# Optimization experiments

Hardware: AMD Instinct MI355X
Metric: run time of the kernel (lower is better)

The kernel has to match this reference:

```python
import jax, jax.numpy as jnp
import numpy as np

D_MODEL = 1024
N_HEADS = 16
D_HEAD = D_MODEL // N_HEADS
HIDDEN = 4 * D_MODEL
EPS = 1e-5
ROPE_BASE = 10000.0


def layernorm(x, g, b):
    mu = jnp.mean(x, axis=-1, keepdims=True)
    var = jnp.mean((x - mu) ** 2, axis=-1, keepdims=True)
    return (x - mu) * jax.lax.rsqrt(var + EPS) * g + b


def rope(t, pos):
    # t: (B, N, D), pos: (N,) int -> rotary transform over D (half-split pairs)
    half = t.shape[-1] // 2
    inv_freq = 1.0 / (ROPE_BASE ** (jnp.arange(half, dtype=jnp.float32) / half))
    ang = pos.astype(jnp.float32)[:, None] * inv_freq  # (N, half)
    cos, sin = jnp.cos(ang), jnp.sin(ang)
    t1, t2 = t[..., :half], t[..., half:]
    return jnp.concatenate([t1 * cos - t2 * sin, t1 * sin + t2 * cos], axis=-1)


def setup_inputs() -> dict:
    key = jax.random.key(0)
    ks = jax.random.split(key, 12)
    B, N, D, H = 2, 2048, D_MODEL, HIDDEN
    s = 0.02
    return {
        "x": jax.random.normal(ks[0], (B, N, D), jnp.float32),
        "pos": jnp.arange(N, dtype=jnp.int32),
        "Wq": jax.random.normal(ks[1], (D, D), jnp.float32) * s,
        "bq": jnp.zeros((D,), jnp.float32),
        "Wk": jax.random.normal(ks[2], (D, D), jnp.float32) * s,
        "bk": jnp.zeros((D,), jnp.float32),
        "Wv": jax.random.normal(ks[3], (D, D), jnp.float32) * s,
        "bv": jnp.zeros((D,), jnp.float32),
        "Wo": jax.random.normal(ks[4], (D, D), jnp.float32) * s,
        "bo": jnp.zeros((D,), jnp.float32),
        "g1": jnp.ones((D,), jnp.float32),
        "b1": jnp.zeros((D,), jnp.float32),
        "g2": jnp.ones((D,), jnp.float32),
        "b2": jnp.zeros((D,), jnp.float32),
        "W1": jax.random.normal(ks[5], (D, H), jnp.float32) * s,
        "bm1": jnp.zeros((H,), jnp.float32),
        "W2": jax.random.normal(ks[6], (H, D), jnp.float32) * s,
        "bm2": jnp.zeros((D,), jnp.float32),
    }


def reference(x, pos, Wq, bq, Wk, bk, Wv, bv, Wo, bo, g1, b1, g2, b2, W1, bm1, W2, bm2):
    B, N, D = x.shape
    Hh, dh = N_HEADS, D_HEAD

    # --- attention sublayer (pre-norm) ---
    h = layernorm(x, g1, b1)
    q = h @ Wq + bq
    k = h @ Wk + bk
    v = h @ Wv + bv
    q = rope(q, pos)
    k = rope(k, pos)
    # split heads: (B, Hh, N, dh)
    q = q.reshape(B, N, Hh, dh).transpose(0, 2, 1, 3)
    k = k.reshape(B, N, Hh, dh).transpose(0, 2, 1, 3)
    v = v.reshape(B, N, Hh, dh).transpose(0, 2, 1, 3)
    scores = jnp.einsum("bhqd,bhkd->bhqk", q, k) / jnp.sqrt(jnp.float32(dh))
    attn = jax.nn.softmax(scores, axis=-1)
    ctx = jnp.einsum("bhqk,bhkd->bhqd", attn, v)
    ctx = ctx.transpose(0, 2, 1, 3).reshape(B, N, D)
    x = x + ctx @ Wo + bo

    # --- MLP sublayer (pre-norm, exact GELU) ---
    h = layernorm(x, g2, b2)
    h = jax.nn.gelu(h @ W1 + bm1, approximate=False)
    x = x + h @ W2 + bm2
    return x
```

## Files before the change

kernel.cpp:

```cpp
#include <hip/hip_runtime.h>

typedef __bf16 bf16x8 __attribute__((ext_vector_type(8)));
typedef __bf16 bf16x4 __attribute__((ext_vector_type(4)));
typedef float  f32x4  __attribute__((ext_vector_type(4)));

#define D_MODEL 1024
#define SEQ     2048
#define BATCH   2
#define NH      16
#define DH      64
#define HID     4096
#define ROWS    (BATCH*SEQ)

static __device__ __forceinline__ void gl_lds16(const __bf16* g, __bf16* l) {
  __builtin_amdgcn_global_load_lds(
      (const __attribute__((address_space(1))) unsigned int*)g,
      (__attribute__((address_space(3))) unsigned int*)l, 16, 0, 0);
}

__global__ __launch_bounds__(256) void ln_kernel(
    const float* __restrict__ x, const float* __restrict__ g,
    const float* __restrict__ b, __bf16* __restrict__ out)
{
  int row = blockIdx.x;
  const float* xr = x + (size_t)row * D_MODEL;
  int i0 = threadIdx.x * 4;
  f32x4 xv = *(const f32x4*)(xr + i0);
  float s  = xv[0] + xv[1] + xv[2] + xv[3];
  float ss = xv[0]*xv[0] + xv[1]*xv[1] + xv[2]*xv[2] + xv[3]*xv[3];
#pragma unroll
  for (int off = 1; off < 64; off <<= 1) {
    s  += __shfl_xor(s,  off, 64);
    ss += __shfl_xor(ss, off, 64);
  }
  __shared__ float red[8];
  int wave = threadIdx.x >> 6;
  if ((threadIdx.x & 63) == 0) { red[wave] = s; red[4 + wave] = ss; }
  __syncthreads();
  s  = red[0] + red[1] + red[2] + red[3];
  ss = red[4] + red[5] + red[6] + red[7];
  float mu  = s * (1.0f / D_MODEL);
  float var = ss * (1.0f / D_MODEL) - mu * mu;
  float inv = rsqrtf(var + 1e-5f);
  f32x4 gv = *(const f32x4*)(g + i0);
  f32x4 bv = *(const f32x4*)(b + i0);
  bf16x4 ov;
#pragma unroll
  for (int j = 0; j < 4; ++j)
    ov[j] = (__bf16)((xv[j] - mu) * inv * gv[j] + bv[j]);
  *(bf16x4*)(out + (size_t)row * D_MODEL + i0) = ov;
}

__global__ __launch_bounds__(256) void convT_kernel(
    const float* __restrict__ W, __bf16* __restrict__ Wt, int K, int N)
{
  __shared__ float T[32][33];
  int n0 = blockIdx.x * 32, k0 = blockIdx.y * 32;
  int r  = threadIdx.x >> 3;
  int c4 = (threadIdx.x & 7) * 4;
  f32x4 v = *(const f32x4*)(W + (size_t)(k0 + r) * N + n0 + c4);
#pragma unroll
  for (int i = 0; i < 4; ++i) T[r][c4 + i] = v[i];
  __syncthreads();
  bf16x4 o;
#pragma unroll
  for (int i = 0; i < 4; ++i) o[i] = (__bf16)T[c4 + i][r];
  *(bf16x4*)(Wt + (size_t)(n0 + r) * K + k0 + c4) = o;
}

__global__ void biascat_kernel(const float* __restrict__ a,
                               const float* __restrict__ b,
                               const float* __restrict__ c,
                               float* __restrict__ o)
{
  int i = blockIdx.x * 256 + threadIdx.x;
  o[i] = i < 1024 ? a[i] : (i < 2048 ? b[i - 1024] : c[i - 2048]);
}

__global__ __launch_bounds__(256) void gemm128(
    const __bf16* __restrict__ A, const __bf16* __restrict__ Bt,
    const float* __restrict__ bias, const float* __restrict__ resid,
    void* __restrict__ Cv, int M, int N, int K, int act, int c_fp32)
{
  __shared__ __bf16 As[128 * 64];
  __shared__ __bf16 Bs[128 * 64];
  int tid = threadIdx.x, lane = tid & 63, wv = tid >> 6;
  int quad = lane >> 4, l16 = lane & 15;
  int wr = wv >> 1, wc = wv & 1;
  int gx = M >> 7, gy = N >> 7;
  int blk = blockIdx.x;
  int xcd = blk & 7, t = blk >> 3;
  int row0 = (t % gx) * 128;
  int col0 = (xcd * (gy >> 3) + t / gx) * 128;
  int s_r8 = lane >> 3;
  int s_c8 = lane & 7;
  int s_src = (s_c8 ^ s_r8) * 8;
  int sw = l16 & 7;
  f32x4 acc[4][4] = {};

  for (int k0 = 0; k0 < K; k0 += 64) {
#pragma unroll
    for (int p = 0; p < 4; ++p) {
      int r = p * 32 + wv * 8 + s_r8;
      gl_lds16(A  + (size_t)(row0 + r) * K + k0 + s_src, As + p * 2048 + wv * 512);
      gl_lds16(Bt + (size_t)(col0 + r) * K + k0 + s_src, Bs + p * 2048 + wv * 512);
    }
    __syncthreads();
#pragma unroll
    for (int kk = 0; kk < 2; ++kk) {
      int slot = ((kk * 4 + quad) ^ sw) * 8;
      bf16x8 af[4], bf[4];
#pragma unroll
      for (int i = 0; i < 4; ++i) {
        af[i] = *(const bf16x8*)(As + (wr * 64 + i * 16 + l16) * 64 + slot);
        bf[i] = *(const bf16x8*)(Bs + (wc * 64 + i * 16 + l16) * 64 + slot);
      }
#pragma unroll
      for (int i = 0; i < 4; ++i)
#pragma unroll
        for (int j = 0; j < 4; ++j)
          acc[i][j] = __builtin_amdgcn_mfma_f32_16x16x32_bf16(af[i], bf[j], acc[i][j], 0, 0, 0);
    }
    __syncthreads();
  }
#pragma unroll
  for (int i = 0; i < 4; ++i) {
    int grow = row0 + wr * 64 + i * 16 + quad * 4;
#pragma unroll
    for (int j = 0; j < 4; ++j) {
      int gcol = col0 + wc * 64 + j * 16 + l16;
      float bsv = bias[gcol];
#pragma unroll
      for (int r = 0; r < 4; ++r) {
        size_t off = (size_t)(grow + r) * N + gcol;
        float v = acc[i][j][r] + bsv;
        if (act) v = 0.5f * v * (1.0f + erff(v * 0.70710678118654752f));
        if (resid) v += resid[off];
        if (c_fp32) ((float*)Cv)[off] = v;
        else        ((__bf16*)Cv)[off] = (__bf16)v;
      }
    }
  }
}

__global__ __launch_bounds__(256) void gemm64x128(
    const __bf16* __restrict__ A, const __bf16* __restrict__ Bt,
    const float* __restrict__ bias, const float* __restrict__ resid,
    void* __restrict__ Cv, int M, int N, int K, int act, int c_fp32)
{
  __shared__ __bf16 As[64 * 64];
  __shared__ __bf16 Bs[128 * 64];
  int tid = threadIdx.x, lane = tid & 63, wv = tid >> 6;
  int quad = lane >> 4, l16 = lane & 15;
  int wr = wv >> 1, wc = wv & 1;
  int gx = M >> 6, gy = N >> 7;
  int blk = blockIdx.x;
  int xcd = blk & 7, t = blk >> 3;
  int row0 = (t % gx) * 64;
  int col0 = (xcd * (gy >> 3) + t / gx) * 128;
  int s_r8 = lane >> 3;
  int s_c8 = lane & 7;
  int s_src = (s_c8 ^ s_r8) * 8;
  int sw = l16 & 7;
  f32x4 acc[2][4] = {};

  for (int k0 = 0; k0 < K; k0 += 64) {
#pragma unroll
    for (int p = 0; p < 4; ++p) {
      int r = p * 32 + wv * 8 + s_r8;
      if (p < 2)
        gl_lds16(A + (size_t)(row0 + r) * K + k0 + s_src, As + p * 2048 + wv * 512);
      gl_lds16(Bt + (size_t)(col0 + r) * K + k0 + s_src, Bs + p * 2048 + wv * 512);
    }
    __syncthreads();
#pragma unroll
    for (int kk = 0; kk < 2; ++kk) {
      int slot = ((kk * 4 + quad) ^ sw) * 8;
      bf16x8 af[2], bf[4];
#pragma unroll
      for (int i = 0; i < 2; ++i)
        af[i] = *(const bf16x8*)(As + (wr * 32 + i * 16 + l16) * 64 + slot);
#pragma unroll
      for (int j = 0; j < 4; ++j)
        bf[j] = *(const bf16x8*)(Bs + (wc * 64 + j * 16 + l16) * 64 + slot);
#pragma unroll
      for (int i = 0; i < 2; ++i)
#pragma unroll
        for (int j = 0; j < 4; ++j)
          acc[i][j] = __builtin_amdgcn_mfma_f32_16x16x32_bf16(af[i], bf[j], acc[i][j], 0, 0, 0);
    }
    __syncthreads();
  }
#pragma unroll
  for (int i = 0; i < 2; ++i) {
    int grow = row0 + wr * 32 + i * 16 + quad * 4;
#pragma unroll
    for (int j = 0; j < 4; ++j) {
      int gcol = col0 + wc * 64 + j * 16 + l16;
      float bsv = bias[gcol];
#pragma unroll
      for (int r = 0; r < 4; ++r) {
        size_t off = (size_t)(grow + r) * N + gcol;
        float v = acc[i][j][r] + bsv;
        if (act) v = 0.5f * v * (1.0f + erff(v * 0.70710678118654752f));
        if (resid) v += resid[off];
        if (c_fp32) ((float*)Cv)[off] = v;
        else        ((__bf16*)Cv)[off] = (__bf16)v;
      }
    }
  }
}

__global__ __launch_bounds__(256) void rope_repack(
    const __bf16* __restrict__ qkv, const int* __restrict__ pos,
    __bf16* __restrict__ Qh, __bf16* __restrict__ Kh)
{
  int row = blockIdx.x;
  int b = row >> 11, n = row & (SEQ - 1);
  float p = (float)pos[n];
  const __bf16* qr = qkv + (size_t)row * 3072;
#pragma unroll
  for (int t = 0; t < 2; ++t) {
    int i = threadIdx.x + t * 256;
    float fr  = expf(-9.210340371976184f * ((float)i * (1.0f / 512.0f)));
    float ang = p * fr;
    float sn, c;
    sincosf(ang, &sn, &c);
    float q1 = (float)qr[i],        q2 = (float)qr[512 + i];
    float k1 = (float)qr[1024 + i], k2 = (float)qr[1536 + i];
    int h1 = i >> 6, d1 = i & 63;
    int h2 = (i + 512) >> 6;
    size_t o1 = ((size_t)(b * NH + h1) * SEQ + n) * DH + d1;
    size_t o2 = ((size_t)(b * NH + h2) * SEQ + n) * DH + d1;
    Qh[o1] = (__bf16)((q1 * c - q2 * sn) * 0.125f);
    Qh[o2] = (__bf16)((q1 * sn + q2 * c) * 0.125f);
    Kh[o1] = (__bf16)(k1 * c - k2 * sn);
    Kh[o2] = (__bf16)(k1 * sn + k2 * c);
  }
}

__global__ __launch_bounds__(256) void vtrans_kernel(
    const __bf16* __restrict__ Vsrc, int vstride, __bf16* __restrict__ Vt,
    int blocked)
{
  __shared__ __bf16 T[64][72];
  int bh = blockIdx.x;
  int kb = blockIdx.y * 64;
  int b = bh >> 4, h = bh & 15;
  int tid = threadIdx.x;
#pragma unroll
  for (int t = 0; t < 2; ++t) {
    int u = tid + t * 256;
    int r = u >> 3, seg = (u & 7) * 8;
    bf16x8 v = *(const bf16x8*)(Vsrc + (size_t)(b * SEQ + kb + r) * vstride + h * DH + seg);
    *(bf16x8*)(&T[r][seg]) = v;
  }
  __syncthreads();
#pragma unroll
  for (int t = 0; t < 2; ++t) {
    int u = tid + t * 256;
    int d = u >> 3, ks = (u & 7) * 8;
    bf16x8 o;
#pragma unroll
    for (int i = 0; i < 8; ++i) o[i] = T[ks + i][d];
    if (blocked) {
      int key = kb + ks;
      *(bf16x8*)(Vt + (((size_t)bh * (SEQ / 128) + (key >> 7)) * DH + d) * 128 + (key & 127)) = o;
    } else {
      *(bf16x8*)(Vt + ((size_t)bh * DH + d) * SEQ + kb + ks) = o;
    }
  }
}

#define KS 136
__global__ __launch_bounds__(256) void attn_split(
    const __bf16* __restrict__ Qh, const __bf16* __restrict__ Kh,
    const __bf16* __restrict__ Vt, __bf16* __restrict__ pacc,
    float* __restrict__ pml)
{
  __shared__ __bf16 Ks[128 * 64];
  __shared__ __bf16 Vs[64 * 128];
  __shared__ __bf16 Pl[4][16 * KS];
  int tid = threadIdx.x, lane = tid & 63, wave = tid >> 6;
  int quad = lane >> 4, l16 = lane & 15;
  int blk = blockIdx.x;
  int split = blk >> 10;
  int rr = blk & 1023;
  int bh  = ((rr & 7) << 2) | ((rr >> 3) & 3);
  int q64 = rr >> 5;
  int q0 = q64 * 64 + wave * 16;
  const __bf16* qbase = Qh + (size_t)bh * SEQ * DH;
  const __bf16* kbase = Kh + (size_t)bh * SEQ * DH;
  const __bf16* vbase = Vt + (size_t)bh * SEQ * DH;
  const __bf16* qp = qbase + (size_t)(q0 + l16) * DH + quad * 8;
  bf16x8 qf0 = *(const bf16x8*)(qp);
  bf16x8 qf1 = *(const bf16x8*)(qp + 32);
  float lrow[4] = {0.f, 0.f, 0.f, 0.f};
  f32x4 acc[4] = {};
  __bf16* pw = &Pl[wave][0];
  int s_kr = lane >> 3;
  int s_k8 = lane & 7;
  int s_vd = lane >> 4;
  int s_vs = lane & 15;
  int sw8  = l16 & 7;

  int kb0 = split * (SEQ / 2);
  for (int it = 0; it < (SEQ / 2) / 128; ++it) {
    int kb = kb0 + it * 128;
    const __bf16* kt = kbase + (size_t)kb * DH;
    const __bf16* vt = vbase + (size_t)(kb >> 7) * (DH * 128);
    __syncthreads();
#pragma unroll
    for (int p = 0; p < 4; ++p) {
      int key0 = p * 32 + wave * 8;
      int swz  = (key0 >> 3) & 7;
      gl_lds16(kt + (key0 + s_kr) * DH + ((s_k8 ^ swz) * 8), Ks + p * 2048 + wave * 512);
      int d = p * 16 + wave * 4 + s_vd;
      gl_lds16(vt + d * 128 + ((s_vs ^ (d & 15)) * 8), Vs + p * 2048 + wave * 512);
    }
    __syncthreads();
    f32x4 s[8];
#pragma unroll
    for (int j = 0; j < 8; ++j) {
      const __bf16* kr = Ks + (l16 * 8 + j) * 64;
      bf16x8 kf0 = *(const bf16x8*)(kr + (quad ^ sw8) * 8);
      bf16x8 kf1 = *(const bf16x8*)(kr + ((quad ^ sw8) ^ 4) * 8);
      f32x4 z = {};
      z = __builtin_amdgcn_mfma_f32_16x16x32_bf16(qf0, kf0, z, 0, 0, 0);
      s[j] = __builtin_amdgcn_mfma_f32_16x16x32_bf16(qf1, kf1, z, 0, 0, 0);
    }
#pragma unroll
    for (int r = 0; r < 4; ++r) {
      bf16x8 pv;
      float rs = 0.f;
#pragma unroll
      for (int j = 0; j < 8; ++j) {
        float pj = __expf(s[j][r]);
        rs += pj;
        pv[j] = (__bf16)pj;
      }
      lrow[r] += rs;
      *(bf16x8*)(pw + (quad * 4 + r) * KS + l16 * 8) = pv;
    }
#pragma unroll
    for (int kk = 0; kk < 4; ++kk) {
      bf16x8 pf = *(const bf16x8*)(pw + l16 * KS + kk * 32 + quad * 8);
#pragma unroll
      for (int j = 0; j < 4; ++j) {
        int d = j * 16 + l16;
        bf16x8 vf = *(const bf16x8*)(Vs + d * 128 + (((kk * 4 + quad) ^ (d & 15)) * 8));
        acc[j] = __builtin_amdgcn_mfma_f32_16x16x32_bf16(pf, vf, acc[j], 0, 0, 0);
      }
    }
  }
#pragma unroll
  for (int r = 0; r < 4; ++r)
#pragma unroll
    for (int off = 1; off < 16; off <<= 1) lrow[r] += __shfl_xor(lrow[r], off, 64);
#pragma unroll
  for (int r = 0; r < 4; ++r) {
    int brow = wave * 16 + quad * 4 + r;
#pragma unroll
    for (int j = 0; j < 4; ++j)
      pacc[((size_t)blk * 64 + brow) * 64 + j * 16 + l16] = (__bf16)acc[j][r];
    if (l16 == 0) {
      pml[(size_t)blk * 128 + brow]      = 0.f;
      pml[(size_t)blk * 128 + 64 + brow] = lrow[r];
    }
  }
}

__global__ __launch_bounds__(256) void attn_combine(
    const __bf16* __restrict__ pacc, const float* __restrict__ pml,
    __bf16* __restrict__ ctx)
{
  int bq = blockIdx.x;
  int q64 = bq & 31, bh = bq >> 5;
  int b = bh >> 4, h = bh & 15;
  int tid = threadIdx.x;
  int r = tid >> 2;
  int c = (tid & 3) * 16;
  int blk0 = ((q64 * 4 + (bh & 3)) << 3) | (bh >> 2);
  int blk1 = blk0 + 1024;
  float m0 = pml[(size_t)blk0 * 128 + r], l0 = pml[(size_t)blk0 * 128 + 64 + r];
  float m1 = pml[(size_t)blk1 * 128 + r], l1 = pml[(size_t)blk1 * 128 + 64 + r];
  float m = fmaxf(m0, m1);
  float w0 = __expf(m0 - m), w1 = __expf(m1 - m);
  float inv = 1.0f / (w0 * l0 + w1 * l1);
  size_t r0 = ((size_t)blk0 * 64 + r) * 64 + c;
  size_t r1 = ((size_t)blk1 * 64 + r) * 64 + c;
  size_t ob = ((size_t)(b * SEQ) + q64 * 64 + r) * D_MODEL + h * DH + c;
#pragma unroll
  for (int g = 0; g < 2; ++g) {
    bf16x8 a0 = *(const bf16x8*)(pacc + r0 + g * 8);
    bf16x8 a1 = *(const bf16x8*)(pacc + r1 + g * 8);
    bf16x8 o;
#pragma unroll
    for (int i = 0; i < 8; ++i)
      o[i] = (__bf16)((w0 * (float)a0[i] + w1 * (float)a1[i]) * inv);
    *(bf16x8*)(ctx + ob + g * 8) = o;
  }
}

__global__ __launch_bounds__(256) void rope_inplace(
    __bf16* __restrict__ ql, __bf16* __restrict__ kl,
    const int* __restrict__ pos, int stride)
{
  int row = blockIdx.x;
  int n = row & (SEQ - 1);
  float p = (float)pos[n];
  const size_t rbase = (size_t)row * stride;
#pragma unroll
  for (int t = 0; t < 2; ++t) {
    int i = threadIdx.x + t * 256;
    float fr  = expf(-9.210340371976184f * ((float)i * (1.0f / 512.0f)));
    float ang = p * fr;
    float sn, c;
    sincosf(ang, &sn, &c);
    float q1 = (float)ql[rbase + i], q2 = (float)ql[rbase + 512 + i];
    float k1 = (float)kl[rbase + i], k2 = (float)kl[rbase + 512 + i];
    ql[rbase + i]       = (__bf16)(q1 * c - q2 * sn);
    ql[rbase + 512 + i] = (__bf16)(q1 * sn + q2 * c);
    kl[rbase + i]       = (__bf16)(k1 * c - k2 * sn);
    kl[rbase + 512 + i] = (__bf16)(k1 * sn + k2 * c);
  }
}

__global__ __launch_bounds__(256) void attn_kernel(
    const __bf16* __restrict__ Q, const __bf16* __restrict__ K,
    const __bf16* __restrict__ Vt, __bf16* __restrict__ ctx, int qkstride)
{
  __shared__ __bf16 Pl[4][16 * KS];
  int tid = threadIdx.x, lane = tid & 63, wave = tid >> 6;
  int quad = lane >> 4, l16 = lane & 15;
  int blk = blockIdx.x;
  int q64 = blk & 31;
  int bh  = blk >> 5;
  int b = bh >> 4, h = bh & 15;
  int q0 = q64 * 64 + wave * 16;
  const __bf16* qbase = Q + (size_t)b * SEQ * qkstride + h * DH;
  const __bf16* kbase = K + (size_t)b * SEQ * qkstride + h * DH;
  const __bf16* vbase = Vt + (size_t)bh * DH * SEQ;
  const __bf16* qp = qbase + (size_t)(q0 + l16) * qkstride + quad * 8;
  bf16x8 qf0 = *(const bf16x8*)(qp);
  bf16x8 qf1 = *(const bf16x8*)(qp + 32);
  float mrow[4] = {-1e30f, -1e30f, -1e30f, -1e30f};
  float lrow[4] = {0.f, 0.f, 0.f, 0.f};
  f32x4 acc[4] = {};
  __bf16* pw = &Pl[wave][0];

  for (int kb = 0; kb < SEQ; kb += 128) {
    f32x4 s[8];
#pragma unroll
    for (int j = 0; j < 8; ++j) {
      const __bf16* kp = kbase + (size_t)(kb + l16 * 8 + j) * qkstride + quad * 8;
      bf16x8 kf0 = *(const bf16x8*)(kp);
      bf16x8 kf1 = *(const bf16x8*)(kp + 32);
      f32x4 z = {};
      z = __builtin_amdgcn_mfma_f32_16x16x32_bf16(qf0, kf0, z, 0, 0, 0);
      z = __builtin_amdgcn_mfma_f32_16x16x32_bf16(qf1, kf1, z, 0, 0, 0);
#pragma unroll
      for (int r = 0; r < 4; ++r) s[j][r] = z[r] * 0.125f;
    }
#pragma unroll
    for (int r = 0; r < 4; ++r) {
      float mx = s[0][r];
#pragma unroll
      for (int j = 1; j < 8; ++j) mx = fmaxf(mx, s[j][r]);
#pragma unroll
      for (int off = 1; off < 16; off <<= 1) mx = fmaxf(mx, __shfl_xor(mx, off, 64));
      float mn = fmaxf(mrow[r], mx);
      float al = __expf(mrow[r] - mn);
      float p[8], rs = 0.f;
#pragma unroll
      for (int j = 0; j < 8; ++j) { p[j] = __expf(s[j][r] - mn); rs += p[j]; }
#pragma unroll
      for (int off = 1; off < 16; off <<= 1) rs += __shfl_xor(rs, off, 64);
      lrow[r] = lrow[r] * al + rs;
      mrow[r] = mn;
#pragma unroll
      for (int j = 0; j < 4; ++j) acc[j][r] *= al;
      bf16x8 pv;
#pragma unroll
      for (int j = 0; j < 8; ++j) pv[j] = (__bf16)p[j];
      *(bf16x8*)(pw + (quad * 4 + r) * KS + l16 * 8) = pv;
    }
#pragma unroll
    for (int kk = 0; kk < 4; ++kk) {
      bf16x8 pf = *(const bf16x8*)(pw + l16 * KS + kk * 32 + quad * 8);
#pragma unroll
      for (int j = 0; j < 4; ++j) {
        bf16x8 vf = *(const bf16x8*)(vbase + (size_t)(j * 16 + l16) * SEQ + kb + kk * 32 + quad * 8);
        acc[j] = __builtin_amdgcn_mfma_f32_16x16x32_bf16(pf, vf, acc[j], 0, 0, 0);
      }
    }
  }
#pragma unroll
  for (int r = 0; r < 4; ++r) {
    int row = q0 + quad * 4 + r;
    float inv = 1.0f / lrow[r];
    size_t obase = ((size_t)(b * SEQ) + row) * D_MODEL + h * DH;
#pragma unroll
    for (int j = 0; j < 4; ++j)
      ctx[obase + j * 16 + l16] = (__bf16)(acc[j][r] * inv);
  }
}

extern "C" void kernel_launch(void* const* d_in, const int* in_sizes, int n_in,
                              void* d_out, int out_size, void* d_ws, size_t ws_size,
                              hipStream_t stream)
{
  const float* x   = (const float*)d_in[0];
  const int*   pos = (const int*)  d_in[1];
  const float* Wq  = (const float*)d_in[2];
  const float* bq  = (const float*)d_in[3];
  const float* Wk  = (const float*)d_in[4];
  const float* bk  = (const float*)d_in[5];
  const float* Wv  = (const float*)d_in[6];
  const float* bv  = (const float*)d_in[7];
  const float* Wo  = (const float*)d_in[8];
  const float* bo  = (const float*)d_in[9];
  const float* g1  = (const float*)d_in[10];
  const float* b1  = (const float*)d_in[11];
  const float* g2  = (const float*)d_in[12];
  const float* b2  = (const float*)d_in[13];
  const float* W1  = (const float*)d_in[14];
  const float* bm1 = (const float*)d_in[15];
  const float* W2  = (const float*)d_in[16];
  const float* bm2 = (const float*)d_in[17];
  float* out = (float*)d_out;

  const size_t MB = 1024 * 1024;
  char* w = (char*)d_ws;
  dim3 blk(256);
  dim3 gConvD(D_MODEL / 32, D_MODEL / 32);
  dim3 gConv1(HID / 32, D_MODEL / 32);
  dim3 gConv2(D_MODEL / 32, HID / 32);
  dim3 gVt(BATCH * NH, SEQ / 64);

  if (ws_size >= (size_t)96 * MB) {
    __bf16* hln   = (__bf16*)(w + 0 * MB);
    float*  x1    = (float*) (w + 8 * MB);
    __bf16* qkv   = (__bf16*)(w + 24 * MB);
    __bf16* pacc  = (__bf16*)(w + 24 * MB);
    float*  pml   = (float*) (w + 41 * MB);
    __bf16* hmlp  = (__bf16*)(w + 24 * MB);
    __bf16* Qh    = (__bf16*)(w + 48 * MB);
    __bf16* ctx   = (__bf16*)(w + 48 * MB);
    __bf16* Kh    = (__bf16*)(w + 56 * MB);
    __bf16* W2T   = (__bf16*)(w + 56 * MB);
    __bf16* Vt    = (__bf16*)(w + 64 * MB);
    __bf16* W1T   = (__bf16*)(w + 64 * MB);
    __bf16* WqkvT = (__bf16*)(w + 72 * MB);
    __bf16* WoT   = (__bf16*)(w + 78 * MB);
    float*  bqkv  = (float*) (w + 80 * MB);

    convT_kernel<<<gConvD, blk, 0, stream>>>(Wq, WqkvT,               D_MODEL, D_MODEL);
    convT_kernel<<<gConvD, blk, 0, stream>>>(Wk, WqkvT + 1024 * 1024, D_MODEL, D_MODEL);
    convT_kernel<<<gConvD, blk, 0, stream>>>(Wv, WqkvT + 2048 * 1024, D_MODEL, D_MODEL);
    convT_kernel<<<gConvD, blk, 0, stream>>>(Wo, WoT, D_MODEL, D_MODEL);
    biascat_kernel<<<12, blk, 0, stream>>>(bq, bk, bv, bqkv);
    ln_kernel<<<ROWS, blk, 0, stream>>>(x, g1, b1, hln);
    gemm128<<<(ROWS / 128) * (3072 / 128), blk, 0, stream>>>(hln, WqkvT, bqkv, nullptr, qkv, ROWS, 3072, D_MODEL, 0, 0);
    rope_repack<<<ROWS, blk, 0, stream>>>(qkv, pos, Qh, Kh);
    vtrans_kernel<<<gVt, blk, 0, stream>>>(qkv + 2048, 3072, Vt, 1);
    attn_split<<<BATCH * NH * (SEQ / 64) * 2, blk, 0, stream>>>(Qh, Kh, Vt, pacc, pml);
    attn_combine<<<BATCH * NH * (SEQ / 64), blk, 0, stream>>>(pacc, pml, ctx);
    convT_kernel<<<gConv1, blk, 0, stream>>>(W1, W1T, D_MODEL, HID);
    convT_kernel<<<gConv2, blk, 0, stream>>>(W2, W2T, HID, D_MODEL);
    gemm64x128<<<(ROWS / 64) * (D_MODEL / 128), blk, 0, stream>>>(ctx, WoT, bo, x, x1, ROWS, D_MODEL, D_MODEL, 0, 1);
    ln_kernel<<<ROWS, blk, 0, stream>>>(x1, g2, b2, hln);
    gemm128<<<(ROWS / 128) * (HID / 128), blk, 0, stream>>>(hln, W1T, bm1, nullptr, hmlp, ROWS, HID, D_MODEL, 1, 0);
    gemm64x128<<<(ROWS / 64) * (D_MODEL / 128), blk, 0, stream>>>(hmlp, W2T, bm2, x1, out, ROWS, D_MODEL, HID, 0, 1);
  } else {
    __bf16* hln  = (__bf16*)(w + 0 * MB);
    __bf16* vlin = (__bf16*)(w + 8 * MB);
    __bf16* WqT  = (__bf16*)(w + 16 * MB);
    __bf16* WkT  = (__bf16*)(w + 18 * MB);
    __bf16* WvT  = (__bf16*)(w + 20 * MB);
    __bf16* ctx  = (__bf16*)(w + 16 * MB);
    __bf16* WoT  = (__bf16*)(w + 8 * MB);
    __bf16* W1T  = (__bf16*)(w + 8 * MB);
    __bf16* W2T  = (__bf16*)(w + 16 * MB);
    __bf16* Vt   = (__bf16*)(w + 24 * MB);
    __bf16* hmlp = (__bf16*)(w + 24 * MB);
    __bf16* qlin = (__bf16*)d_out;
    __bf16* klin = (__bf16*)d_out + (size_t)ROWS * D_MODEL;
    float*  x1   = (float*)d_out;

    convT_kernel<<<gConvD, blk, 0, stream>>>(Wq, WqT, D_MODEL, D_MODEL);
    convT_kernel<<<gConvD, blk, 0, stream>>>(Wk, WkT, D_MODEL, D_MODEL);
    convT_kernel<<<gConvD, blk, 0, stream>>>(Wv, WvT, D_MODEL, D_MODEL);
    ln_kernel<<<ROWS, blk, 0, stream>>>(x, g1, b1, hln);
    int nLin = (ROWS / 64) * (D_MODEL / 128);
    gemm64x128<<<nLin, blk, 0, stream>>>(hln, WqT, bq, nullptr, qlin, ROWS, D_MODEL, D_MODEL, 0, 0);
    gemm64x128<<<nLin, blk, 0, stream>>>(hln, WkT, bk, nullptr, klin, ROWS, D_MODEL, D_MODEL, 0, 0);
    gemm64x128<<<nLin, blk, 0, stream>>>(hln, WvT, bv, nullptr, vlin, ROWS, D_MODEL, D_MODEL, 0, 0);
    rope_inplace<<<ROWS, blk, 0, stream>>>(qlin, klin, pos, D_MODEL);
    vtrans_kernel<<<gVt, blk, 0, stream>>>(vlin, D_MODEL, Vt, 0);
    attn_kernel<<<BATCH * NH * (SEQ / 64), blk, 0, stream>>>(qlin, klin, Vt, ctx, D_MODEL);
    convT_kernel<<<gConvD, blk, 0, stream>>>(Wo, WoT, D_MODEL, D_MODEL);
    gemm64x128<<<nLin, blk, 0, stream>>>(ctx, WoT, bo, x, x1, ROWS, D_MODEL, D_MODEL, 0, 1);
    ln_kernel<<<ROWS, blk, 0, stream>>>(x1, g2, b2, hln);
    convT_kernel<<<gConv1, blk, 0, stream>>>(W1, W1T, D_MODEL, HID);
    convT_kernel<<<gConv2, blk, 0, stream>>>(W2, W2T, HID, D_MODEL);
    const int CH = 1024;
    for (int c = 0; c < ROWS / CH; ++c) {
      const __bf16* a1 = hln + (size_t)c * CH * D_MODEL;
      gemm128<<<(CH / 128) * (HID / 128), blk, 0, stream>>>(a1, W1T, bm1, nullptr, hmlp, CH, HID, D_MODEL, 1, 0);
      gemm64x128<<<(CH / 64) * (D_MODEL / 128), blk, 0, stream>>>(hmlp, W2T, bm2, x1 + (size_t)c * CH * D_MODEL,
                                          out + (size_t)c * CH * D_MODEL, CH, D_MODEL, HID, 0, 1);
    }
  }
}
```

Before: 438.4 us.

## Add double-buffered 256x256 GEMM kernel for QKV and MLP projections

Introduces a 512-thread GEMM with 256x256 output tiles, double-buffered LDS staging through direct global-to-LDS loads, and a chiplet-aware block remapping. The QKV, W1 and W2 projections now use it instead of the 128-tile kernels. Larger tiles raise operand reuse and cut global traffic, while the double buffering overlaps loads with MFMA work. The cost is fewer workgroups: the W2 GEMM launches only 64 blocks on a 256-CU device, which underfills the machine. High register use from 32 accumulators per thread may also limit occupancy.

```diff
diff --git a/kernel.cpp b/kernel.cpp
--- a/kernel.cpp
+++ b/kernel.cpp
@@ -75,6 +75,94 @@
 {
   int i = blockIdx.x * 256 + threadIdx.x;
   o[i] = i < 1024 ? a[i] : (i < 2048 ? b[i - 1024] : c[i - 2048]);
+}
+
+__global__ __launch_bounds__(512, 2) void gemm256(
+    const __bf16* __restrict__ A, const __bf16* __restrict__ Bt,
+    const float* __restrict__ bias, const float* __restrict__ resid,
+    void* __restrict__ Cv, int M, int N, int K, int act, int c_fp32)
+{
+  __shared__ __bf16 As[2][256 * 64];
+  __shared__ __bf16 Bs[2][256 * 64];
+  int tid = threadIdx.x, lane = tid & 63, wv = tid >> 6;
+  int quad = lane >> 4, l16 = lane & 15;
+  int wr = wv >> 2, wc = wv & 3;
+  int gx = M >> 8, gy = N >> 8;
+  int nwg = gx * gy;
+  int xcd = blockIdx.x & 7;
+  int q = nwg >> 3, r8 = nwg & 7;
+  int wg = (xcd < r8 ? xcd * (q + 1) : r8 * (q + 1) + (xcd - r8) * q) + (blockIdx.x >> 3);
+  int row0 = (wg % gx) << 8;
+  int col0 = (wg / gx) << 8;
+  int s_r  = lane >> 3;
+  int s_src = ((lane & 7) ^ s_r) * 8;
+  int sw = l16 & 7;
+  int NT = K >> 6;
+  f32x4 acc[8][4] = {};
+
+#define G256_STAGE(kt, b)                                                     \
+  {                                                                           \
+    int k0_ = (kt) * 64;                                                      \
+    _Pragma("unroll")                                                         \
+    for (int rd = 0; rd < 4; ++rd) {                                          \
+      int rrow = rd * 64 + wv * 8 + s_r;                                      \
+      gl_lds16(A  + (size_t)(row0 + rrow) * K + k0_ + s_src,                  \
+               &As[b][rd * 4096 + wv * 512]);                                 \
+      gl_lds16(Bt + (size_t)(col0 + rrow) * K + k0_ + s_src,                  \
+               &Bs[b][rd * 4096 + wv * 512]);                                 \
+    }                                                                         \
+  }
+
+  G256_STAGE(0, 0);
+  G256_STAGE(1, 1);
+
+  for (int t = 0; t < NT; ++t) {
+    if (t + 1 < NT) asm volatile("s_waitcnt vmcnt(8)" ::: "memory");
+    else            asm volatile("s_waitcnt vmcnt(0)" ::: "memory");
+    __builtin_amdgcn_s_barrier();
+    const __bf16* Ab = &As[t & 1][0];
+    const __bf16* Bb = &Bs[t & 1][0];
+    __builtin_amdgcn_s_setprio(1);
+#pragma unroll
+    for (int kk = 0; kk < 2; ++kk) {
+      int slot = ((kk * 4 + quad) ^ sw) * 8;
+      bf16x8 bfr[4];
+#pragma unroll
+      for (int j = 0; j < 4; ++j)
+        bfr[j] = *(const bf16x8*)(Bb + (wc * 64 + j * 16 + l16) * 64 + slot);
+      bf16x8 afr[8];
+#pragma unroll
+      for (int i = 0; i < 8; ++i)
+        afr[i] = *(const bf16x8*)(Ab + (wr * 128 + i * 16 + l16) * 64 + slot);
+#pragma unroll
+      for (int i = 0; i < 8; ++i)
+#pragma unroll
+        for (int j = 0; j < 4; ++j)
+          acc[i][j] = __builtin_amdgcn_mfma_f32_16x16x32_bf16(afr[i], bfr[j], acc[i][j], 0, 0, 0);
+    }
+    __builtin_amdgcn_s_setprio(0);
+    __builtin_amdgcn_s_barrier();
+    if (t + 2 < NT) G256_STAGE(t + 2, t & 1);
+  }
+
+#pragma unroll
+  for (int i = 0; i < 8; ++i) {
+    int grow = row0 + wr * 128 + i * 16 + quad * 4;
+#pragma unroll
+    for (int j = 0; j < 4; ++j) {
+      int gcol = col0 + wc * 64 + j * 16 + l16;
+      float bsv = bias[gcol];
+#pragma unroll
+      for (int r = 0; r < 4; ++r) {
+        size_t off = (size_t)(grow + r) * N + gcol;
+        float v = acc[i][j][r] + bsv;
+        if (act) v = 0.5f * v * (1.0f + erff(v * 0.70710678118654752f));
+        if (resid) v += resid[off];
+        if (c_fp32) ((float*)Cv)[off] = v;
+        else        ((__bf16*)Cv)[off] = (__bf16)v;
+      }
+    }
+  }
 }
 
 __global__ __launch_bounds__(256) void gemm128(
@@ -533,6 +621,7 @@
   const size_t MB = 1024 * 1024;
   char* w = (char*)d_ws;
   dim3 blk(256);
+  dim3 blk512(512);
   dim3 gConvD(D_MODEL / 32, D_MODEL / 32);
   dim3 gConv1(HID / 32, D_MODEL / 32);
   dim3 gConv2(D_MODEL / 32, HID / 32);
@@ -561,7 +650,7 @@
     convT_kernel<<<gConvD, blk, 0, stream>>>(Wo, WoT, D_MODEL, D_MODEL);
     biascat_kernel<<<12, blk, 0, stream>>>(bq, bk, bv, bqkv);
     ln_kernel<<<ROWS, blk, 0, stream>>>(x, g1, b1, hln);
-    gemm128<<<(ROWS / 128) * (3072 / 128), blk, 0, stream>>>(hln, WqkvT, bqkv, nullptr, qkv, ROWS, 3072, D_MODEL, 0, 0);
+    gemm256<<<(ROWS / 256) * (3072 / 256), blk512, 0, stream>>>(hln, WqkvT, bqkv, nullptr, qkv, ROWS, 3072, D_MODEL, 0, 0);
     rope_repack<<<ROWS, blk, 0, stream>>>(qkv, pos, Qh, Kh);
     vtrans_kernel<<<gVt, blk, 0, stream>>>(qkv + 2048, 3072, Vt, 1);
     attn_split<<<BATCH * NH * (SEQ / 64) * 2, blk, 0, stream>>>(Qh, Kh, Vt, pacc, pml);
@@ -570,8 +659,8 @@
     convT_kernel<<<gConv2, blk, 0, stream>>>(W2, W2T, HID, D_MODEL);
     gemm64x128<<<(ROWS / 64) * (D_MODEL / 128), blk, 0, stream>>>(ctx, WoT, bo, x, x1, ROWS, D_MODEL, D_MODEL, 0, 1);
     ln_kernel<<<ROWS, blk, 0, stream>>>(x1, g2, b2, hln);
-    gemm128<<<(ROWS / 128) * (HID / 128), blk, 0, stream>>>(hln, W1T, bm1, nullptr, hmlp, ROWS, HID, D_MODEL, 1, 0);
-    gemm64x128<<<(ROWS / 64) * (D_MODEL / 128), blk, 0, stream>>>(hmlp, W2T, bm2, x1, out, ROWS, D_MODEL, HID, 0, 1);
+    gemm256<<<(ROWS / 256) * (HID / 256), blk512, 0, stream>>>(hln, W1T, bm1, nullptr, hmlp, ROWS, HID, D_MODEL, 1, 0);
+    gemm256<<<(ROWS / 256) * (D_MODEL / 256), blk512, 0, stream>>>(hmlp, W2T, bm2, x1, out, ROWS, D_MODEL, HID, 0, 1);
   } else {
     __bf16* hln  = (__bf16*)(w + 0 * MB);
     __bf16* vlin = (__bf16*)(w + 8 * MB);
```

Result: slower. 514.9 us (+17.4%).
